# Optimization experiments

Measured on AMD Instinct MI355X. Metric: run time of the kernel, lower is better.

Reference implementation:

```python
import jax, jax.numpy as jnp
import numpy as np

H = 128
N = 1024


def _layernorm(x, g, b, eps=1e-5):
    m = x.mean(-1, keepdims=True)
    v = x.var(-1, keepdims=True)  # biased variance, matches torch LayerNorm
    return (x - m) / jnp.sqrt(v + eps) * g + b


def setup_inputs() -> dict:
    key = jax.random.key(0)
    ks = jax.random.split(key, 16)
    w = lambda k, shp: (jax.random.normal(k, shp, dtype=jnp.float32) * 0.05)
    return {
        "embeddings": jax.random.normal(ks[0], (N, H), dtype=jnp.float32),
        "trace_feats": jax.random.uniform(ks[1], (N, 5), dtype=jnp.float32),
        # consolidation_network: Linear(2H,H) -> LN -> GELU -> Linear(H,H//2) -> GELU -> Linear(H//2,1) -> Sigmoid
        "cW1": w(ks[2], (2 * H, H)), "cb1": jnp.zeros((H,), jnp.float32),
        "ln_g": jnp.ones((H,), jnp.float32), "ln_b": jnp.zeros((H,), jnp.float32),
        "cW2": w(ks[3], (H, H // 2)), "cb2": jnp.zeros((H // 2,), jnp.float32),
        "cW3": w(ks[4], (H // 2, 1)), "cb3": jnp.zeros((1,), jnp.float32),
        # association_generator: Linear(2H,H) -> ReLU -> Linear(H,H//4) -> ReLU -> Linear(H//4,1) -> Sigmoid
        "aW1": w(ks[5], (2 * H, H)), "ab1": jnp.zeros((H,), jnp.float32),
        "aW2": w(ks[6], (H, H // 4)), "ab2": jnp.zeros((H // 4,), jnp.float32),
        "aW3": w(ks[7], (H // 4, 1)), "ab3": jnp.zeros((1,), jnp.float32),
        # importance_predictor: Linear(H+5,H//2) -> GELU -> Linear(H//2,1) -> Sigmoid
        "iW1": w(ks[8], (H + 5, H // 2)), "ib1": jnp.zeros((H // 2,), jnp.float32),
        "iW2": w(ks[9], (H // 2, 1)), "ib2": jnp.zeros((1,), jnp.float32),
    }


def reference(embeddings, trace_feats,
              cW1, cb1, ln_g, ln_b, cW2, cb2, cW3, cb3,
              aW1, ab1, aW2, ab2, aW3, ab3,
              iW1, ib1, iW2, ib2):
    n = embeddings.shape[0]
    gelu = lambda x: jax.nn.gelu(x, approximate=False)  # torch nn.GELU default (erf)
    # All ordered pairs i < j, batched in one pass (replaces the O(N^2) Python loop).
    ii, jj = jnp.triu_indices(n, k=1)                    # [P], P = N(N-1)/2
    pair = jnp.concatenate([embeddings[ii], embeddings[jj]], axis=-1)  # [P, 2H]
    # consolidation scores
    h = gelu(_layernorm(pair @ cW1 + cb1, ln_g, ln_b))   # [P, H]
    h = gelu(h @ cW2 + cb2)                               # [P, H//2]
    cons = jax.nn.sigmoid(h @ cW3 + cb3)[:, 0]           # [P]
    # association strengths
    a = jax.nn.relu(pair @ aW1 + ab1)                     # [P, H]
    a = jax.nn.relu(a @ aW2 + ab2)                        # [P, H//4]
    assoc = jax.nn.sigmoid(a @ aW3 + ab3)[:, 0]          # [P]
    # future importance per trace
    fin = jnp.concatenate([embeddings, trace_feats], axis=-1)  # [N, H+5]
    imp = jax.nn.sigmoid(gelu(fin @ iW1 + ib1) @ iW2 + ib2)[:, 0]  # [N]
    return jnp.concatenate([cons, assoc, imp])           # [2P + N]
```

## Files before the change

### kernel.cpp

```cpp
#include <hip/hip_runtime.h>

#define N_TR 1024
#define H_DIM 128
#define P_PAIRS 523776
#define TI 8
#define N_BLOCKS 1088
#define WS_U    0
#define WS_V    131072
#define WS_SUMU 393216
#define WS_SUMV 395264
#define WS_UAH  524288
#define WS_VAH  655360
#define WS_FRAG_BYTES 1589248u

typedef __attribute__((ext_vector_type(8))) short bf16x8;
typedef __attribute__((ext_vector_type(8))) _Float16 h16x8;
typedef __attribute__((ext_vector_type(4))) float f32x4;

__device__ __forceinline__ short f2bfs(float f) {
  unsigned x = __float_as_uint(f);
  unsigned r = x + 0x7fffu + ((x >> 16) & 1u);
  return (short)(r >> 16);
}
__device__ __forceinline__ unsigned short f2h(float f) {
  _Float16 h = (_Float16)f;
  return __builtin_bit_cast(unsigned short, h);
}
__device__ __forceinline__ unsigned pk_bf16(float f0, float f1) {
  unsigned a0 = __float_as_uint(f0) + 0x8000u;
  unsigned a1 = __float_as_uint(f1) + 0x8000u;
  return __builtin_amdgcn_perm(a1, a0, 0x07060302u);
}
__device__ __forceinline__ float geluf(float x) {
  float u = x * x;
  float p = __builtin_fmaf(u, 0.10294324f, 2.30220820f);
  float e = __builtin_amdgcn_exp2f(x * p);
  float r = __builtin_amdgcn_rcpf(e + 1.0f);
  return __builtin_fmaf(-x, r, x);
}
__device__ __forceinline__ float sigmoidf_(float x) {
  float e = __builtin_amdgcn_exp2f(x * -1.4426950408889634f);
  return __builtin_amdgcn_rcpf(1.0f + e);
}
template <int CTRL>
__device__ __forceinline__ float dpp_add(float x) {
  int v = __builtin_amdgcn_update_dpp(0, __float_as_int(x), CTRL, 0xf, 0xf, true);
  return x + __int_as_float(v);
}
__device__ __forceinline__ float red16(float x) {
  x = dpp_add<0xB1>(x);
  x = dpp_add<0x4E>(x);
  x = dpp_add<0x141>(x);
  x = dpp_add<0x140>(x);
  return x;
}

__global__ __launch_bounds__(256) void k_pre(
    const float* __restrict__ emb, const float* __restrict__ tf,
    const float* __restrict__ cW1, const float* __restrict__ cb1,
    const float* __restrict__ aW1, const float* __restrict__ ab1,
    const float* __restrict__ cW2, const float* __restrict__ aW2,
    const float* __restrict__ iW1, const float* __restrict__ ib1,
    const float* __restrict__ iW2, const float* __restrict__ ib2,
    float* __restrict__ ws, unsigned short* __restrict__ wsH,
    unsigned short* __restrict__ frag, float* __restrict__ out)
{
  __shared__ __align__(16) float sE[2][128];
  __shared__ float sRed[2][8];
  const int blk = blockIdx.x;
  const int t = threadIdx.x;
  const int lane = t & 63, wave = t >> 6;

  if (blk < 512) {
    const int b = blk;
    { int r = t >> 7, c = t & 127; sE[r][c] = emb[(b * 2 + r) * 128 + c]; }
    __syncthreads();
    const int k = t & 127;
    const bool cons = (t < 128);
    const float* W    = cons ? cW1 : aW1;
    const float* bias = cons ? cb1 : ab1;
    float accU0 = 0.f, accU1 = 0.f, accV0 = 0.f, accV1 = 0.f;
    for (int c = 0; c < 128; ++c) {
      float wt = W[c * 128 + k];
      float wb = W[(128 + c) * 128 + k];
      float e0 = sE[0][c], e1 = sE[1][c];
      accU0 = __builtin_fmaf(e0, wt, accU0);
      accU1 = __builtin_fmaf(e1, wt, accU1);
      accV0 = __builtin_fmaf(e0, wb, accV0);
      accV1 = __builtin_fmaf(e1, wb, accV1);
    }
    const float bv = bias[k];
    const float vb0 = accV0 + bv, vb1 = accV1 + bv;
    if (cons) {
      ws[WS_U + (b * 2 + 0) * 128 + k] = accU0;
      ws[WS_U + (b * 2 + 1) * 128 + k] = accU1;
      ws[WS_V + (b * 2 + 0) * 128 + k] = vb0;
      ws[WS_V + (b * 2 + 1) * 128 + k] = vb1;
      float vals[8] = {accU0, accU0 * accU0, accU1, accU1 * accU1,
                       vb0, vb0 * vb0, vb1, vb1 * vb1};
      #pragma unroll
      for (int msk = 1; msk <= 32; msk <<= 1)
        #pragma unroll
        for (int v = 0; v < 8; ++v) vals[v] += __shfl_xor(vals[v], msk, 64);
      if ((t & 63) == 0)
        #pragma unroll
        for (int v = 0; v < 8; ++v) sRed[t >> 6][v] = vals[v];
    } else {
      wsH[WS_UAH + (b * 2 + 0) * 128 + k] = f2h(accU0);
      wsH[WS_UAH + (b * 2 + 1) * 128 + k] = f2h(accU1);
      wsH[WS_VAH + (b * 2 + 0) * 128 + k] = f2h(vb0);
      wsH[WS_VAH + (b * 2 + 1) * 128 + k] = f2h(vb1);
    }
    __syncthreads();
    if (t == 0) {
      const int i0 = b * 2;
      ws[WS_SUMU + i0 * 2 + 0]       = sRed[0][0] + sRed[1][0];
      ws[WS_SUMU + i0 * 2 + 1]       = sRed[0][1] + sRed[1][1];
      ws[WS_SUMU + (i0 + 1) * 2 + 0] = sRed[0][2] + sRed[1][2];
      ws[WS_SUMU + (i0 + 1) * 2 + 1] = sRed[0][3] + sRed[1][3];
      ws[WS_SUMV + i0 * 2 + 0]       = sRed[0][4] + sRed[1][4];
      ws[WS_SUMV + i0 * 2 + 1]       = sRed[0][5] + sRed[1][5];
      ws[WS_SUMV + (i0 + 1) * 2 + 0] = sRed[0][6] + sRed[1][6];
      ws[WS_SUMV + (i0 + 1) * 2 + 1] = sRed[0][7] + sRed[1][7];
    }
  } else if (blk < 560) {
    int u = (blk - 512) * 256 + t;
    if (u < 8192) {
      int j = u & 7, ln = (u >> 3) & 63, ks = (u >> 9) & 3, nt = u >> 11;
      frag[u] = (unsigned short)f2bfs(cW2[(ks * 32 + (ln >> 4) * 8 + j) * 64 + nt * 16 + (ln & 15)]);
    } else {
      int v = u - 8192;
      int j = v & 7, ln = (v >> 3) & 63, ks = (v >> 9) & 3, nt = v >> 11;
      frag[u] = f2h(aW2[(ks * 32 + (ln >> 4) * 8 + j) * 32 + nt * 16 + (ln & 15)]);
    }
  } else {
    const int r = (blk - 560) * 4 + wave;
    float acc = 0.f;
    for (int c = 0; c < 128; ++c)
      acc = __builtin_fmaf(emb[r * 128 + c], iW1[c * 64 + lane], acc);
    #pragma unroll
    for (int c = 0; c < 5; ++c)
      acc = __builtin_fmaf(tf[r * 5 + c], iW1[(128 + c) * 64 + lane], acc);
    float d = geluf(acc + ib1[lane]) * iW2[lane];
    #pragma unroll
    for (int msk = 32; msk; msk >>= 1) d += __shfl_xor(d, msk, 64);
    if (lane == 0) out[2 * P_PAIRS + r] = sigmoidf_(d + ib2[0]);
  }
}

__global__ __launch_bounds__(256, 4) void k_pairs(
    const float* __restrict__ ws, const unsigned short* __restrict__ wsH,
    const unsigned short* __restrict__ frag,
    const float* __restrict__ lng, const float* __restrict__ lnb,
    const float* __restrict__ cb2, const float* __restrict__ cW3,
    const float* __restrict__ cb3,
    const float* __restrict__ ab2, const float* __restrict__ aW3,
    const float* __restrict__ ab3,
    float* __restrict__ out)
{
  __shared__ __align__(16) unsigned short sFrag[12288];
  __shared__ __align__(16) float sU[TI][128];
  __shared__ __align__(16) unsigned short sUaH[TI][128];
  __shared__ __align__(16) float sG[128];
  __shared__ __align__(16) float sB[128];
  __shared__ float sSt[TI * 2];
  const int t = threadIdx.x;

  const int b = blockIdx.x;
  int jt = (int)((sqrtf((float)b + 1.0f) - 1.0f) * 0.5f);
  while (4 * (jt + 1) * (jt + 2) <= b) ++jt;
  while (jt > 0 && 4 * jt * (jt + 1) > b) --jt;
  const int i0 = (b - 4 * jt * (jt + 1)) * TI;

  {
    const uint4* src = (const uint4*)frag;
    uint4* dst = (uint4*)sFrag;
    #pragma unroll
    for (int q = 0; q < 6; ++q) dst[t + q * 256] = src[t + q * 256];
  }
  {
    int r = t >> 5, c4 = (t & 31) * 4;
    *(float4*)&sU[r][c4] = *(const float4*)(ws + WS_U + (i0 + r) * 128 + c4);
    *(ushort4*)&sUaH[r][c4] = *(const ushort4*)(wsH + WS_UAH + (i0 + r) * 128 + c4);
  }
  if (t < 128) { sG[t] = lng[t]; sB[t] = lnb[t]; }
  if (t < TI * 2) sSt[t] = ws[WS_SUMU + i0 * 2 + t];
  __syncthreads();

  const int lane = t & 63;
  const int wave = t >> 6;
  const int m = lane & 15;
  const int g = lane >> 4;
  const int j = jt * 64 + wave * 16 + m;
  const float* Vrow = ws + WS_V + j * 128;
  const float svj = ws[WS_SUMV + j * 2];
  const float qvj = ws[WS_SUMV + j * 2 + 1];

  float vC[4][8];
  h16x8 vAh[4];
  #pragma unroll
  for (int ks = 0; ks < 4; ++ks) {
    const int off = ks * 32 + g * 8;
    float4 a0 = *(const float4*)(Vrow + off);
    float4 a1 = *(const float4*)(Vrow + off + 4);
    vC[ks][0]=a0.x; vC[ks][1]=a0.y; vC[ks][2]=a0.z; vC[ks][3]=a0.w;
    vC[ks][4]=a1.x; vC[ks][5]=a1.y; vC[ks][6]=a1.z; vC[ks][7]=a1.w;
    vAh[ks] = *(const h16x8*)(wsH + WS_VAH + j * 128 + off);
  }

  float cb2v[4], cw3v[4], ab2v[2], aw3v[2];
  #pragma unroll
  for (int nt = 0; nt < 4; ++nt) { cb2v[nt] = cb2[nt * 16 + m]; cw3v[nt] = cW3[nt * 16 + m]; }
  #pragma unroll
  for (int nt = 0; nt < 2; ++nt) { ab2v[nt] = ab2[nt * 16 + m]; aw3v[nt] = aW3[nt * 16 + m]; }
  const float cb3s = cb3[0], ab3s = ab3[0];
  const bf16x8* bfr  = (const bf16x8*)sFrag;
  const h16x8*  bfrA = (const h16x8*)sFrag + 1024;
  const f32x4 zero = {0.f, 0.f, 0.f, 0.f};
  const h16x8 hzero = {0, 0, 0, 0, 0, 0, 0, 0};
  const float inv128 = 0.0078125f;

  for (int it = 0; it < TI; ++it) {
    const int i = i0 + it;
    if (jt * 64 + wave * 16 + 15 <= i) continue;

    const float* su_row = sU[it];

    float xc[4][8];
    float d = 0.f;
    #pragma unroll
    for (int ks = 0; ks < 4; ++ks) {
      const int off = ks * 32 + g * 8;
      float4 u0 = *(const float4*)(su_row + off);
      float4 u1 = *(const float4*)(su_row + off + 4);
      float us[8] = {u0.x,u0.y,u0.z,u0.w,u1.x,u1.y,u1.z,u1.w};
      #pragma unroll
      for (int s = 0; s < 8; ++s) {
        xc[ks][s] = us[s] + vC[ks][s];
        d = __builtin_fmaf(us[s], vC[ks][s], d);
      }
    }
    d += __shfl_xor(d, 16, 64);
    d += __shfl_xor(d, 32, 64);

    h16x8 pA[4];
    #pragma unroll
    for (int ks = 0; ks < 4; ++ks) {
      const int off = ks * 32 + g * 8;
      h16x8 ua = *(const h16x8*)&sUaH[it][off];
      pA[ks] = __builtin_elementwise_max(ua + vAh[ks], hzero);
    }

    const float su = sSt[it * 2], qu = sSt[it * 2 + 1];
    const float mean = (su + svj) * inv128;
    const float ex2  = __builtin_fmaf(2.f, d, qu + qvj) * inv128;
    const float var  = ex2 - mean * mean;
    const float rstd = rsqrtf(var + 1e-5f);

    int4 pC[4];
    #pragma unroll
    for (int ks = 0; ks < 4; ++ks) {
      const int off = ks * 32 + g * 8;
      float4 g0 = *(const float4*)(sG + off);
      float4 g1 = *(const float4*)(sG + off + 4);
      float4 b0 = *(const float4*)(sB + off);
      float4 b1 = *(const float4*)(sB + off + 4);
      float gg[8] = {g0.x,g0.y,g0.z,g0.w,g1.x,g1.y,g1.z,g1.w};
      float bb[8] = {b0.x,b0.y,b0.z,b0.w,b1.x,b1.y,b1.z,b1.w};
      float y[8];
      #pragma unroll
      for (int s = 0; s < 8; ++s) {
        float tq = (xc[ks][s] - mean) * rstd;
        y[s] = geluf(__builtin_fmaf(tq, gg[s], bb[s]));
      }
      pC[ks].x = pk_bf16(y[0], y[1]); pC[ks].y = pk_bf16(y[2], y[3]);
      pC[ks].z = pk_bf16(y[4], y[5]); pC[ks].w = pk_bf16(y[6], y[7]);
    }

    f32x4 accC[4] = {zero, zero, zero, zero};
    f32x4 accA[2] = {zero, zero};
    #pragma unroll
    for (int ks = 0; ks < 4; ++ks) {
      bf16x8 aC = __builtin_bit_cast(bf16x8, pC[ks]);
      #pragma unroll
      for (int nt = 0; nt < 4; ++nt)
        accC[nt] = __builtin_amdgcn_mfma_f32_16x16x32_bf16(
            aC, bfr[(nt * 4 + ks) * 64 + lane], accC[nt], 0, 0, 0);
      #pragma unroll
      for (int nt = 0; nt < 2; ++nt)
        accA[nt] = __builtin_amdgcn_mfma_f32_16x16x32_f16(
            pA[ks], bfrA[(nt * 4 + ks) * 64 + lane], accA[nt], 0, 0, 0);
    }

    float sc[4] = {0.f, 0.f, 0.f, 0.f};
    float sa[4] = {0.f, 0.f, 0.f, 0.f};
    #pragma unroll
    for (int nt = 0; nt < 4; ++nt)
      #pragma unroll
      for (int r = 0; r < 4; ++r)
        sc[r] = __builtin_fmaf(geluf(accC[nt][r] + cb2v[nt]), cw3v[nt], sc[r]);
    #pragma unroll
    for (int nt = 0; nt < 2; ++nt)
      #pragma unroll
      for (int r = 0; r < 4; ++r)
        sa[r] = __builtin_fmaf(fmaxf(accA[nt][r] + ab2v[nt], 0.f), aw3v[nt], sa[r]);
    #pragma unroll
    for (int r = 0; r < 4; ++r) { sc[r] = red16(sc[r]); sa[r] = red16(sa[r]); }

    if (m < 4) {
      const int jr = jt * 64 + wave * 16 + g * 4 + m;
      if (jr > i) {
        const int p = i * (2 * N_TR - i - 1) / 2 + (jr - i - 1);
        out[p]           = sigmoidf_(sc[m] + cb3s);
        out[P_PAIRS + p] = sigmoidf_(sa[m] + ab3s);
      }
    }
  }
}

extern "C" void kernel_launch(void* const* d_in, const int* in_sizes, int n_in,
                              void* d_out, int out_size, void* d_ws, size_t ws_size,
                              hipStream_t stream) {
  const float* emb = (const float*)d_in[0];
  const float* tf  = (const float*)d_in[1];
  const float* cW1 = (const float*)d_in[2];
  const float* cb1 = (const float*)d_in[3];
  const float* lng = (const float*)d_in[4];
  const float* lnb = (const float*)d_in[5];
  const float* cW2 = (const float*)d_in[6];
  const float* cb2 = (const float*)d_in[7];
  const float* cW3 = (const float*)d_in[8];
  const float* cb3 = (const float*)d_in[9];
  const float* aW1 = (const float*)d_in[10];
  const float* ab1 = (const float*)d_in[11];
  const float* aW2 = (const float*)d_in[12];
  const float* ab2 = (const float*)d_in[13];
  const float* aW3 = (const float*)d_in[14];
  const float* ab3 = (const float*)d_in[15];
  const float* iW1 = (const float*)d_in[16];
  const float* ib1 = (const float*)d_in[17];
  const float* iW2 = (const float*)d_in[18];
  const float* ib2 = (const float*)d_in[19];

  float* ws = (float*)d_ws;
  unsigned short* wsH = (unsigned short*)d_ws;
  unsigned short* frag = (unsigned short*)((char*)d_ws + WS_FRAG_BYTES);
  float* out = (float*)d_out;

  hipLaunchKernelGGL(k_pre, dim3(816), dim3(256), 0, stream,
                     emb, tf, cW1, cb1, aW1, ab1, cW2, aW2,
                     iW1, ib1, iW2, ib2, ws, wsH, frag, out);
  hipLaunchKernelGGL(k_pairs, dim3(N_BLOCKS), dim3(256), 0, stream,
                     ws, wsH, frag, lng, lnb, cb2, cW3, cb3, ab2, aW3, ab3, out);
}
```

Measured before the change: 172.8 us.

## Rebalance pair work into evenly split row units across 1024 blocks

Replaces the fixed 8-row by 64-column tiling with a flat list of (column-tile, row) units. Each of 1024 blocks takes a contiguous slice of 8 or 9 units and reloads the V columns only when its slice crosses into a new column tile. The grid now matches four resident blocks per CU with no tail wave, and the padded rows of the old 8-row rounding are no longer processed. The LayerNorm normalisation is also folded into a single FMA. The cost is per-unit index decoding in shared memory and occasional mid-block V reloads.

```diff
diff --git a/kernel.cpp b/kernel.cpp
--- a/kernel.cpp
+++ b/kernel.cpp
@@ -3,8 +3,8 @@
 #define N_TR 1024
 #define H_DIM 128
 #define P_PAIRS 523776
-#define TI 8
-#define N_BLOCKS 1088
+#define N_UNITS 8688
+#define MAX_SLOTS 9
 #define WS_U    0
 #define WS_V    131072
 #define WS_SUMU 393216
@@ -53,6 +53,14 @@
   x = dpp_add<0x141>(x);
   x = dpp_add<0x140>(x);
   return x;
+}
+__device__ __forceinline__ int jt_from_u(int u) {
+  float f = (sqrtf(961.0f + 128.0f * (float)u) - 31.0f) * 0.015625f;
+  int jt = (int)f;
+  if (jt > 15) jt = 15;
+  while (jt < 15 && 32 * (jt + 1) * (jt + 1) + 31 * (jt + 1) <= u) ++jt;
+  while (jt > 0 && 32 * jt * jt + 31 * jt > u) --jt;
+  return jt;
 }
 
 __global__ __launch_bounds__(256) void k_pre(
@@ -159,18 +167,17 @@
     float* __restrict__ out)
 {
   __shared__ __align__(16) unsigned short sFrag[12288];
-  __shared__ __align__(16) float sU[TI][128];
-  __shared__ __align__(16) unsigned short sUaH[TI][128];
+  __shared__ __align__(16) float sU[MAX_SLOTS][128];
+  __shared__ __align__(16) unsigned short sUaH[MAX_SLOTS][128];
   __shared__ __align__(16) float sG[128];
   __shared__ __align__(16) float sB[128];
-  __shared__ float sSt[TI * 2];
+  __shared__ float sSt[MAX_SLOTS * 2];
+  __shared__ int sJt[MAX_SLOTS], sI[MAX_SLOTS];
   const int t = threadIdx.x;
-
   const int b = blockIdx.x;
-  int jt = (int)((sqrtf((float)b + 1.0f) - 1.0f) * 0.5f);
-  while (4 * (jt + 1) * (jt + 2) <= b) ++jt;
-  while (jt > 0 && 4 * jt * (jt + 1) > b) --jt;
-  const int i0 = (b - 4 * jt * (jt + 1)) * TI;
+  const int u0 = (543 * b) >> 6;
+  const int u1 = (543 * (b + 1)) >> 6;
+  const int n  = u1 - u0;
 
   {
     const uint4* src = (const uint4*)frag;
@@ -178,35 +185,34 @@
     #pragma unroll
     for (int q = 0; q < 6; ++q) dst[t + q * 256] = src[t + q * 256];
   }
-  {
-    int r = t >> 5, c4 = (t & 31) * 4;
-    *(float4*)&sU[r][c4] = *(const float4*)(ws + WS_U + (i0 + r) * 128 + c4);
-    *(ushort4*)&sUaH[r][c4] = *(const ushort4*)(wsH + WS_UAH + (i0 + r) * 128 + c4);
+  if (t < n) {
+    int u = u0 + t;
+    int jtu = jt_from_u(u);
+    sJt[t] = jtu;
+    sI[t]  = u - (32 * jtu * jtu + 31 * jtu);
+  }
+  for (int s = t >> 5; s < n; s += 8) {
+    int u = u0 + s;
+    int jtu = jt_from_u(u);
+    int iu = u - (32 * jtu * jtu + 31 * jtu);
+    int c4 = (t & 31) * 4;
+    *(float4*)&sU[s][c4] = *(const float4*)(ws + WS_U + iu * 128 + c4);
+    *(ushort4*)&sUaH[s][c4] = *(const ushort4*)(wsH + WS_UAH + iu * 128 + c4);
+  }
+  if (t < 2 * n) {
+    int s = t >> 1;
+    int u = u0 + s;
+    int jtu = jt_from_u(u);
+    int iu = u - (32 * jtu * jtu + 31 * jtu);
+    sSt[t] = ws[WS_SUMU + iu * 2 + (t & 1)];
   }
   if (t < 128) { sG[t] = lng[t]; sB[t] = lnb[t]; }
-  if (t < TI * 2) sSt[t] = ws[WS_SUMU + i0 * 2 + t];
   __syncthreads();
 
   const int lane = t & 63;
   const int wave = t >> 6;
   const int m = lane & 15;
   const int g = lane >> 4;
-  const int j = jt * 64 + wave * 16 + m;
-  const float* Vrow = ws + WS_V + j * 128;
-  const float svj = ws[WS_SUMV + j * 2];
-  const float qvj = ws[WS_SUMV + j * 2 + 1];
-
-  float vC[4][8];
-  h16x8 vAh[4];
-  #pragma unroll
-  for (int ks = 0; ks < 4; ++ks) {
-    const int off = ks * 32 + g * 8;
-    float4 a0 = *(const float4*)(Vrow + off);
-    float4 a1 = *(const float4*)(Vrow + off + 4);
-    vC[ks][0]=a0.x; vC[ks][1]=a0.y; vC[ks][2]=a0.z; vC[ks][3]=a0.w;
-    vC[ks][4]=a1.x; vC[ks][5]=a1.y; vC[ks][6]=a1.z; vC[ks][7]=a1.w;
-    vAh[ks] = *(const h16x8*)(wsH + WS_VAH + j * 128 + off);
-  }
 
   float cb2v[4], cw3v[4], ab2v[2], aw3v[2];
   #pragma unroll
@@ -220,24 +226,46 @@
   const h16x8 hzero = {0, 0, 0, 0, 0, 0, 0, 0};
   const float inv128 = 0.0078125f;
 
-  for (int it = 0; it < TI; ++it) {
-    const int i = i0 + it;
-    if (jt * 64 + wave * 16 + 15 <= i) continue;
-
-    const float* su_row = sU[it];
+  int jt_cur = -1;
+  float svj = 0.f, qvj = 0.f;
+  float vC[4][8];
+  h16x8 vAh[4];
+
+  for (int s = 0; s < n; ++s) {
+    const int jtu = sJt[s];
+    const int i   = sI[s];
+    if (jtu != jt_cur) {
+      jt_cur = jtu;
+      const int j = jtu * 64 + wave * 16 + m;
+      const float* Vrow = ws + WS_V + j * 128;
+      #pragma unroll
+      for (int ks = 0; ks < 4; ++ks) {
+        const int off = ks * 32 + g * 8;
+        float4 a0 = *(const float4*)(Vrow + off);
+        float4 a1 = *(const float4*)(Vrow + off + 4);
+        vC[ks][0]=a0.x; vC[ks][1]=a0.y; vC[ks][2]=a0.z; vC[ks][3]=a0.w;
+        vC[ks][4]=a1.x; vC[ks][5]=a1.y; vC[ks][6]=a1.z; vC[ks][7]=a1.w;
+        vAh[ks] = *(const h16x8*)(wsH + WS_VAH + j * 128 + off);
+      }
+      svj = ws[WS_SUMV + j * 2];
+      qvj = ws[WS_SUMV + j * 2 + 1];
+    }
+    if (jt_cur * 64 + wave * 16 + 15 <= i) continue;
+
+    const float* su_row = sU[s];
 
     float xc[4][8];
     float d = 0.f;
     #pragma unroll
     for (int ks = 0; ks < 4; ++ks) {
       const int off = ks * 32 + g * 8;
-      float4 u0 = *(const float4*)(su_row + off);
-      float4 u1 = *(const float4*)(su_row + off + 4);
-      float us[8] = {u0.x,u0.y,u0.z,u0.w,u1.x,u1.y,u1.z,u1.w};
-      #pragma unroll
-      for (int s = 0; s < 8; ++s) {
-        xc[ks][s] = us[s] + vC[ks][s];
-        d = __builtin_fmaf(us[s], vC[ks][s], d);
+      float4 u0v = *(const float4*)(su_row + off);
+      float4 u1v = *(const float4*)(su_row + off + 4);
+      float us[8] = {u0v.x,u0v.y,u0v.z,u0v.w,u1v.x,u1v.y,u1v.z,u1v.w};
+      #pragma unroll
+      for (int q = 0; q < 8; ++q) {
+        xc[ks][q] = us[q] + vC[ks][q];
+        d = __builtin_fmaf(us[q], vC[ks][q], d);
       }
     }
     d += __shfl_xor(d, 16, 64);
@@ -247,15 +275,16 @@
     #pragma unroll
     for (int ks = 0; ks < 4; ++ks) {
       const int off = ks * 32 + g * 8;
-      h16x8 ua = *(const h16x8*)&sUaH[it][off];
+      h16x8 ua = *(const h16x8*)&sUaH[s][off];
       pA[ks] = __builtin_elementwise_max(ua + vAh[ks], hzero);
     }
 
-    const float su = sSt[it * 2], qu = sSt[it * 2 + 1];
+    const float su = sSt[s * 2], qu = sSt[s * 2 + 1];
     const float mean = (su + svj) * inv128;
     const float ex2  = __builtin_fmaf(2.f, d, qu + qvj) * inv128;
     const float var  = ex2 - mean * mean;
     const float rstd = rsqrtf(var + 1e-5f);
+    const float nms  = -mean * rstd;
 
     int4 pC[4];
     #pragma unroll
@@ -269,9 +298,9 @@
       float bb[8] = {b0.x,b0.y,b0.z,b0.w,b1.x,b1.y,b1.z,b1.w};
       float y[8];
       #pragma unroll
-      for (int s = 0; s < 8; ++s) {
-        float tq = (xc[ks][s] - mean) * rstd;
-        y[s] = geluf(__builtin_fmaf(tq, gg[s], bb[s]));
+      for (int q = 0; q < 8; ++q) {
+        float tq = __builtin_fmaf(xc[ks][q], rstd, nms);
+        y[q] = geluf(__builtin_fmaf(tq, gg[q], bb[q]));
       }
       pC[ks].x = pk_bf16(y[0], y[1]); pC[ks].y = pk_bf16(y[2], y[3]);
       pC[ks].z = pk_bf16(y[4], y[5]); pC[ks].w = pk_bf16(y[6], y[7]);
@@ -308,7 +337,7 @@
     for (int r = 0; r < 4; ++r) { sc[r] = red16(sc[r]); sa[r] = red16(sa[r]); }
 
     if (m < 4) {
-      const int jr = jt * 64 + wave * 16 + g * 4 + m;
+      const int jr = jt_cur * 64 + wave * 16 + g * 4 + m;
       if (jr > i) {
         const int p = i * (2 * N_TR - i - 1) / 2 + (jr - i - 1);
         out[p]           = sigmoidf_(sc[m] + cb3s);
@@ -350,6 +379,6 @@
   hipLaunchKernelGGL(k_pre, dim3(816), dim3(256), 0, stream,
                      emb, tf, cW1, cb1, aW1, ab1, cW2, aW2,
                      iW1, ib1, iW2, ib2, ws, wsH, frag, out);
-  hipLaunchKernelGGL(k_pairs, dim3(N_BLOCKS), dim3(256), 0, stream,
+  hipLaunchKernelGGL(k_pairs, dim3(1024), dim3(256), 0, stream,
                      ws, wsH, frag, lng, lnb, cb2, cW3, cb3, ab2, aW3, ab3, out);
 }
```

Result: faster. 166.9 us, median of 2 (-3.4%).
